# Kernel optimization log

Hardware: AMD Instinct MI355X
Metric: run time of the kernel (lower is better)

Reference implementation:

```python
import jax, jax.numpy as jnp
import numpy as np

N, E = 50000, 400000
HID, EDGE, NRBF = 128, 16, 32
CUTOFF = 5.0
EPS = 1e-8


def setup_inputs() -> dict:
    key = jax.random.key(0)
    ks = jax.random.split(key, 16)
    s = lambda fan_in: 1.0 / np.sqrt(fan_in)
    mlp_in = 3 * HID + NRBF + EDGE  # 432
    return {
        "h": jax.random.normal(ks[0], (N, HID), jnp.float32),
        "vec": jax.random.normal(ks[1], (N, 3, HID), jnp.float32),
        "coord": jax.random.normal(ks[2], (N, 3), jnp.float32),
        "edge_index": jax.random.randint(ks[3], (2, E), 0, N, jnp.int32),
        "edge_attr": jax.random.normal(ks[4], (E, EDGE), jnp.float32),
        "Wvp": jax.random.normal(ks[5], (HID, 3 * HID), jnp.float32) * s(HID),
        "W1": jax.random.normal(ks[6], (mlp_in, HID), jnp.float32) * s(mlp_in),
        "b1": jnp.zeros((HID,), jnp.float32),
        "W2": jax.random.normal(ks[7], (HID, HID), jnp.float32) * s(HID),
        "b2": jnp.zeros((HID,), jnp.float32),
        "W3": jax.random.normal(ks[8], (HID, 3 * HID), jnp.float32) * s(HID),
        "b3": jnp.zeros((3 * HID,), jnp.float32),
        "Wop": jax.random.normal(ks[9], (HID, 3 * HID), jnp.float32) * s(HID),
        "bop": jnp.zeros((3 * HID,), jnp.float32),
    }


def _rbf(d):
    # Gaussian smearing: centers on linspace(0, cutoff, n_rbf)
    offsets = jnp.linspace(0.0, CUTOFF, NRBF, dtype=d.dtype)
    coeff = -0.5 / (offsets[1] - offsets[0]) ** 2
    return jnp.exp(coeff * (d[:, None] - offsets) ** 2)  # [E, NRBF]


def reference(h, vec, coord, edge_index, edge_attr,
              Wvp, W1, b1, W2, b2, W3, b3, Wop, bop):
    row, col = edge_index[0], edge_index[1]
    x_ij = coord[row] - coord[col]                          # [E,3]
    d = jnp.sqrt(jnp.sum(x_ij * x_ij, axis=-1) + EPS)       # stable_norm
    d_ij = _rbf(d)                                          # [E,NRBF]

    vecp = jnp.einsum('nvh,hk->nvk', vec, Wvp)              # [N,3,3H]
    vec1, vec2, vec3 = jnp.split(vecp, 3, axis=-1)          # each [N,3,H]
    vec_dot = jnp.sum(vec1 * vec2, axis=1)                  # [N,H]

    cross = jnp.sum(vec1[row] * vec2[col], axis=1)          # [E,H]
    mlp_in = jnp.concatenate([h[row], h[col], d_ij, cross, edge_attr], axis=-1)
    x = jax.nn.silu(mlp_in @ W1 + b1)
    x = jax.nn.silu(x @ W2 + b2)
    msg = x @ W3 + b3                                       # [E,3H]
    msg_h, msg_v, msg_x = jnp.split(msg, 3, axis=1)

    h_aggr = jax.ops.segment_sum(msg_h, row, num_segments=N)           # [N,H]
    vec_msg = vec3[col] * msg_v[:, None, :] + msg_x[:, None, :] * x_ij[:, :, None]
    vec_aggr = jax.ops.segment_sum(vec_msg, row, num_segments=N)       # [N,3,H]

    o = h_aggr @ Wop + bop
    o1, o2, o3 = jnp.split(o, 3, axis=1)
    dh = vec_dot * o2 + o3
    dvec = vec3 * o1[:, None, :] + vec_aggr
    return dh, dvec
```

## Files before the change

### kernel.cpp

```cpp
#include <hip/hip_runtime.h>
#include <math.h>

constexpr int NN    = 50000;
constexpr int NE    = 400000;
constexpr int HID   = 128;

constexpr size_t OFF_VECP12 = 0;
constexpr size_t OFF_BUN  = 38400000;
constexpr size_t OFF_HAGG = 64000000;
constexpr size_t OFF_WT   = 83200000;
constexpr size_t OFF_PERM = 83421184;
constexpr size_t OFF_DEG  = 83821184;
constexpr size_t OFF_CUR  = 83871184;
constexpr size_t WS_FLOATS = 83921184;

constexpr size_t O_HWH = 0;
constexpr size_t O_HWL = 32768;
constexpr size_t O_W1H = 65536;
constexpr size_t O_W1L = 90112;
constexpr size_t O_W2H = 114688;
constexpr size_t O_W2L = 131072;
constexpr size_t O_W3H = 147456;
constexpr size_t O_W3L = 196608;
constexpr size_t O_VPH = 245760;
constexpr size_t O_VPL = 294912;
constexpr size_t O_OPH = 344064;
constexpr size_t O_OPL = 393216;

typedef __attribute__((ext_vector_type(8))) short short8;
typedef __attribute__((ext_vector_type(4))) float f32x4;

__device__ __forceinline__ short f2bf_rne(float f) {
    unsigned u = __float_as_uint(f);
    u += 0x7fffu + ((u >> 16) & 1u);
    return (short)(u >> 16);
}
__device__ __forceinline__ float bf2f(short h) {
    return __uint_as_float(((unsigned)(unsigned short)h) << 16);
}
__device__ __forceinline__ void split8(const float* t, short8& ah, short8& al) {
#pragma unroll
    for (int j = 0; j < 8; ++j) {
        short hi = f2bf_rne(t[j]);
        ah[j] = hi;
        al[j] = f2bf_rne(t[j] - bf2f(hi));
    }
}
__device__ __forceinline__ f32x4 mfma4(short8 ah, short8 al, short8 bh, short8 bl, f32x4 c) {
    c = __builtin_amdgcn_mfma_f32_16x16x32_bf16(ah, bh, c, 0, 0, 0);
    c = __builtin_amdgcn_mfma_f32_16x16x32_bf16(al, bh, c, 0, 0, 0);
    c = __builtin_amdgcn_mfma_f32_16x16x32_bf16(ah, bl, c, 0, 0, 0);
    c = __builtin_amdgcn_mfma_f32_16x16x32_bf16(al, bl, c, 0, 0, 0);
    return c;
}

#define VLOAD8(dst, src) do { \
    *(float4*)&(dst)[0] = *(const float4*)(src); \
    *(float4*)&(dst)[4] = *(const float4*)((src) + 4); } while (0)

__global__ void misc_kernel(const float* __restrict__ W1, const float* __restrict__ W2,
                            const float* __restrict__ W3, const float* __restrict__ Wvp,
                            const float* __restrict__ Wop, short* __restrict__ wt,
                            const int* __restrict__ eidx, int* __restrict__ deg,
                            float* __restrict__ hagg, float* __restrict__ dvec)
{
    const int bid = blockIdx.x;
    const int idx = bid * 256 + threadIdx.x;
    {
        int n = idx >> 7, k = idx & 127;
        hagg[idx] = 0.f;
        size_t db = (size_t)n * 384 + k;
        dvec[db] = 0.f; dvec[db + 128] = 0.f; dvec[db + 256] = 0.f;
    }
    if (bid < 864) {
        float v; size_t oh, ol;
        if (idx < 32768) {
            int j = idx >> 7, k = idx & 127;
            v = (j < 128) ? W1[(size_t)k * 128 + j] : W1[(size_t)(128 + k) * 128 + (j - 128)];
            oh = O_HWH + idx; ol = O_HWL + idx;
        } else if (idx < 57344) {
            int l = idx - 32768; int n = l / 192, k = l - n * 192;
            int r = (k < 128) ? (288 + k) : (k < 160) ? (256 + k - 128) : (k < 176) ? (416 + k - 160) : -1;
            v = (r < 0) ? 0.f : W1[(size_t)r * 128 + n];
            oh = O_W1H + l; ol = O_W1L + l;
        } else if (idx < 73728) {
            int l = idx - 57344; int n = l >> 7, k = l & 127;
            v = W2[(size_t)k * 128 + n];
            oh = O_W2H + l; ol = O_W2L + l;
        } else if (idx < 122880) {
            int l = idx - 73728; int n = l >> 7, k = l & 127;
            v = W3[(size_t)k * 384 + n];
            oh = O_W3H + l; ol = O_W3L + l;
        } else if (idx < 172032) {
            int l = idx - 122880; int n = l >> 7, k = l & 127;
            v = Wvp[(size_t)k * 384 + n];
            oh = O_VPH + l; ol = O_VPL + l;
        } else {
            int l = idx - 172032; int n = l >> 7, k = l & 127;
            v = Wop[(size_t)k * 384 + n];
            oh = O_OPH + l; ol = O_OPL + l;
        }
        short hi = f2bf_rne(v);
        wt[oh] = hi;
        wt[ol] = f2bf_rne(v - bf2f(hi));
    }
    if (bid < 1563 && idx < NE)
        atomicAdd(&deg[eidx[idx]], 1);
}

__global__ void __launch_bounds__(1024)
sort_scan(const int* __restrict__ deg, int* __restrict__ cursor)
{
    __shared__ int part[1024];
    const int tid = threadIdx.x;
    const int base = tid * 49;
    int s = 0;
#pragma unroll 7
    for (int j = 0; j < 49; ++j) {
        int i = base + j;
        if (i < NN) s += deg[i];
    }
    part[tid] = s;
    __syncthreads();
    for (int off = 1; off < 1024; off <<= 1) {
        int v = (tid >= off) ? part[tid - off] : 0;
        __syncthreads();
        part[tid] += v;
        __syncthreads();
    }
    int run = part[tid] - s;
    for (int j = 0; j < 49; ++j) {
        int i = base + j;
        if (i < NN) { cursor[i] = run; run += deg[i]; }
    }
}

__global__ void sort_scatter(const int* __restrict__ eidx, int* __restrict__ cursor,
                             int* __restrict__ perm)
{
    int e = blockIdx.x * 256 + threadIdx.x;
    if (e < NE) {
        int pos = atomicAdd(&cursor[eidx[e]], 1);
        perm[pos] = e;
    }
}

__global__ void __launch_bounds__(256, 3)
gemm_vp(const float* __restrict__ A, int M,
        const short* __restrict__ wh, const short* __restrict__ wl,
        float* __restrict__ vecp12, short* __restrict__ bun)
{
    const int tid = threadIdx.x, wave = tid >> 6, lane = tid & 63;
    const int m = lane & 15, kg = lane >> 4;
    const int gm0 = blockIdx.x * 32;
    const int nb = wave * 96;
    const f32x4 zf = {0.f, 0.f, 0.f, 0.f};
    f32x4 acc[2][6];
#pragma unroll
    for (int mt = 0; mt < 2; ++mt)
#pragma unroll
        for (int tt = 0; tt < 6; ++tt) acc[mt][tt] = zf;

    for (int ks = 0; ks < 4; ++ks) {
        short8 ah[2], al[2];
#pragma unroll
        for (int mt = 0; mt < 2; ++mt) {
            int r = gm0 + mt * 16 + m;
            if (r >= M) r = M - 1;
            float tmp[8];
            VLOAD8(tmp, A + (size_t)r * 128 + ks * 32 + kg * 8);
            split8(tmp, ah[mt], al[mt]);
        }
#pragma unroll
        for (int tt = 0; tt < 6; ++tt) {
            size_t wo = (size_t)(nb + tt * 16 + m) * 128 + ks * 32 + kg * 8;
            short8 bh = *(const short8*)(wh + wo);
            short8 bl = *(const short8*)(wl + wo);
#pragma unroll
            for (int mt = 0; mt < 2; ++mt)
                acc[mt][tt] = mfma4(ah[mt], al[mt], bh, bl, acc[mt][tt]);
        }
    }
#pragma unroll
    for (int mt = 0; mt < 2; ++mt)
#pragma unroll
        for (int r = 0; r < 4; ++r) {
            int row = gm0 + mt * 16 + kg * 4 + r;
            if (row >= M) continue;
            int n = row / 3, v = row - n * 3;
            size_t fb = (size_t)n * 768 + (size_t)v * 256;
            size_t b2 = (size_t)n * 1024 + (size_t)v * 128;
            size_t b3 = (size_t)n * 1024 + 384 + (size_t)v * 128;
#pragma unroll
            for (int tt = 0; tt < 6; ++tt) {
                int col = nb + tt * 16 + m;
                float val = acc[mt][tt][r];
                int seg = col >> 7, k = col & 127;
                if (seg == 0) {
                    vecp12[fb + k] = val;
                } else if (seg == 1) {
                    vecp12[fb + 128 + k] = val;
                    bun[b2 + k] = f2bf_rne(val);
                } else {
                    bun[b3 + k] = f2bf_rne(val);
                }
            }
        }
}

__global__ void __launch_bounds__(256, 3)
gemm_hw(const float* __restrict__ A, int M,
        const short* __restrict__ wh, const short* __restrict__ wl,
        short* __restrict__ bun)
{
    const int tid = threadIdx.x, wave = tid >> 6, lane = tid & 63;
    const int m = lane & 15, kg = lane >> 4;
    const int gm0 = blockIdx.x * 32;
    const int nb = wave * 64;
    const f32x4 zf = {0.f, 0.f, 0.f, 0.f};
    f32x4 acc[2][4];
#pragma unroll
    for (int mt = 0; mt < 2; ++mt)
#pragma unroll
        for (int tt = 0; tt < 4; ++tt) acc[mt][tt] = zf;

    for (int ks = 0; ks < 4; ++ks) {
        short8 ah[2], al[2];
#pragma unroll
        for (int mt = 0; mt < 2; ++mt) {
            int r = gm0 + mt * 16 + m;
            if (r >= M) r = M - 1;
            float tmp[8];
            VLOAD8(tmp, A + (size_t)r * 128 + ks * 32 + kg * 8);
            split8(tmp, ah[mt], al[mt]);
        }
#pragma unroll
        for (int tt = 0; tt < 4; ++tt) {
            size_t wo = (size_t)(nb + tt * 16 + m) * 128 + ks * 32 + kg * 8;
            short8 bh = *(const short8*)(wh + wo);
            short8 bl = *(const short8*)(wl + wo);
#pragma unroll
            for (int mt = 0; mt < 2; ++mt)
                acc[mt][tt] = mfma4(ah[mt], al[mt], bh, bl, acc[mt][tt]);
        }
    }
#pragma unroll
    for (int mt = 0; mt < 2; ++mt)
#pragma unroll
        for (int r = 0; r < 4; ++r) {
            int row = gm0 + mt * 16 + kg * 4 + r;
            if (row >= M) continue;
#pragma unroll
            for (int tt = 0; tt < 4; ++tt) {
                int col = nb + tt * 16 + m;
                bun[(size_t)row * 1024 + 768 + col] = f2bf_rne(acc[mt][tt][r]);
            }
        }
}

__global__ void __launch_bounds__(256, 3)
gemm_fin(const float* __restrict__ hagg, const float* __restrict__ vecp12,
         const short* __restrict__ bun,
         const short* __restrict__ wh, const short* __restrict__ wl,
         const float* __restrict__ bop, float* __restrict__ dh,
         float* __restrict__ dvec, int M)
{
    const int tid = threadIdx.x, wave = tid >> 6, lane = tid & 63;
    const int m = lane & 15, kg = lane >> 4;
    const int gm0 = blockIdx.x * 32;
    const int nb = wave * 32;
    const f32x4 zf = {0.f, 0.f, 0.f, 0.f};
    f32x4 acc[2][6];
#pragma unroll
    for (int mt = 0; mt < 2; ++mt)
#pragma unroll
        for (int t = 0; t < 6; ++t) acc[mt][t] = zf;

    for (int ks = 0; ks < 4; ++ks) {
        short8 ah[2], al[2];
#pragma unroll
        for (int mt = 0; mt < 2; ++mt) {
            int r = gm0 + mt * 16 + m;
            if (r >= M) r = M - 1;
            float tmp[8];
            VLOAD8(tmp, hagg + (size_t)r * 128 + ks * 32 + kg * 8);
            split8(tmp, ah[mt], al[mt]);
        }
#pragma unroll
        for (int seg = 0; seg < 3; ++seg)
#pragma unroll
            for (int tt = 0; tt < 2; ++tt) {
                size_t wo = (size_t)(seg * 128 + nb + tt * 16 + m) * 128 + ks * 32 + kg * 8;
                short8 bh = *(const short8*)(wh + wo);
                short8 bl = *(const short8*)(wl + wo);
#pragma unroll
                for (int mt = 0; mt < 2; ++mt)
                    acc[mt][seg * 2 + tt] = mfma4(ah[mt], al[mt], bh, bl, acc[mt][seg * 2 + tt]);
            }
    }
    float bo[3][2];
#pragma unroll
    for (int seg = 0; seg < 3; ++seg)
#pragma unroll
        for (int tt = 0; tt < 2; ++tt) bo[seg][tt] = bop[seg * 128 + nb + tt * 16 + m];

#pragma unroll
    for (int mt = 0; mt < 2; ++mt)
#pragma unroll
        for (int r = 0; r < 4; ++r) {
            int row = gm0 + mt * 16 + kg * 4 + r;
            if (row >= M) continue;
            size_t b = (size_t)row * 768;
            size_t bb = (size_t)row * 1024 + 384;
#pragma unroll
            for (int tt = 0; tt < 2; ++tt) {
                int k = nb + tt * 16 + m;
                float o1 = acc[mt][0 * 2 + tt][r] + bo[0][tt];
                float o2 = acc[mt][1 * 2 + tt][r] + bo[1][tt];
                float o3 = acc[mt][2 * 2 + tt][r] + bo[2][tt];
                float vd = vecp12[b + k]       * vecp12[b + 128 + k]
                         + vecp12[b + 256 + k] * vecp12[b + 384 + k]
                         + vecp12[b + 512 + k] * vecp12[b + 640 + k];
                dh[(size_t)row * 128 + k] = vd * o2 + o3;
                size_t db = (size_t)row * 384 + k;
                dvec[db]       += bf2f(bun[bb + k])       * o1;
                dvec[db + 128] += bf2f(bun[bb + 128 + k]) * o1;
                dvec[db + 256] += bf2f(bun[bb + 256 + k]) * o1;
            }
        }
}

__global__ void __launch_bounds__(256, 4)
edge_kernel(const float* __restrict__ vecp12, const short* __restrict__ bun,
            const float* __restrict__ coord, const int* __restrict__ eidx,
            const float* __restrict__ eattr, const short* __restrict__ wt,
            const int* __restrict__ perm,
            const float* __restrict__ b1, const float* __restrict__ b2,
            const float* __restrict__ b3,
            float* __restrict__ hagg, float* __restrict__ dvec)
{
    __shared__ __align__(16) unsigned char smem[34816];
    short (*xh)[136]  = (short(*)[136])(&smem[0]);
    short (*xl)[136]  = (short(*)[136])(&smem[17408]);
    __shared__ int   s_row[64], s_col[64], s_es[64];
    __shared__ float s_xij[64][3];
    __shared__ float s_d[64];

    const int nwg = gridDim.x;
    const int q8 = nwg >> 3, r8 = nwg & 7;
    const int xcd = blockIdx.x & 7, loc = blockIdx.x >> 3;
    const int lb = (xcd < r8 ? xcd * (q8 + 1) : r8 * (q8 + 1) + (xcd - r8) * q8) + loc;

    const int tid = threadIdx.x;
    const int wave = tid >> 6, lane = tid & 63;
    const int m = lane & 15, kg = lane >> 4;
    const int nb = wave * 32;
    const int eb = lb * 64;
    const int be = tid >> 2;
    const int bq = (tid & 3) * 8;

    if (tid < 64) {
        int es = perm[eb + tid];
        int r = eidx[es], c = eidx[NE + es];
        s_es[tid] = es; s_row[tid] = r; s_col[tid] = c;
        float x0 = coord[r * 3 + 0] - coord[c * 3 + 0];
        float x1 = coord[r * 3 + 1] - coord[c * 3 + 1];
        float x2 = coord[r * 3 + 2] - coord[c * 3 + 2];
        s_xij[tid][0] = x0; s_xij[tid][1] = x1; s_xij[tid][2] = x2;
        s_d[tid] = sqrtf(x0 * x0 + x1 * x1 + x2 * x2 + 1e-8f);
    }
    __syncthreads();

    const f32x4 zf = {0.f, 0.f, 0.f, 0.f};
    const float delta = 5.0f / 31.0f;
    const float coeff = -0.5f / (delta * delta);
    const int brow = s_row[be], bcol = s_col[be], bes = s_es[be];

    float pA[8], pC[8], pE[8];
    short8 bB, bD, bF;
    auto issue = [&](int ks) {
        if (ks < 4) {
            int kk = ks * 32 + bq;
            const float* vr = vecp12 + (size_t)brow * 768 + kk;
            const short* vc = bun + (size_t)bcol * 1024 + kk;
            VLOAD8(pA, vr); VLOAD8(pC, vr + 256); VLOAD8(pE, vr + 512);
            bB = *(const short8*)(vc);
            bD = *(const short8*)(vc + 128);
            bF = *(const short8*)(vc + 256);
        } else if (ks == 5) {
            if (bq < 16) VLOAD8(pA, eattr + (size_t)bes * 16 + bq);
        }
    };
    auto commit = [&](int ks, int buf) {
        short (*cabh)[40] = (short(*)[40])(&smem[(size_t)buf * 5120]);
        short (*cabl)[40] = (short(*)[40])(&smem[10240 + (size_t)buf * 5120]);
        float tmp[8];
        if (ks < 4) {
#pragma unroll
            for (int j = 0; j < 8; ++j)
                tmp[j] = pA[j] * bf2f(bB[j]) + pC[j] * bf2f(bD[j]) + pE[j] * bf2f(bF[j]);
        } else if (ks == 4) {
            float dd = s_d[be];
#pragma unroll
            for (int j = 0; j < 8; ++j) {
                float x = dd - (float)(bq + j) * delta;
                tmp[j] = __expf(coeff * x * x);
            }
        } else {
#pragma unroll
            for (int j = 0; j < 8; ++j) tmp[j] = (bq < 16) ? pA[j] : 0.f;
        }
        short8 sh, sl; split8(tmp, sh, sl);
        *(short8*)&cabh[be][bq] = sh;
        *(short8*)&cabl[be][bq] = sl;
    };

    f32x4 acc[4][2];
#pragma unroll
    for (int mt = 0; mt < 4; ++mt) { acc[mt][0] = zf; acc[mt][1] = zf; }

    issue(0); commit(0, 0);
    __syncthreads();
    for (int ks = 0; ks < 6; ++ks) {
        if (ks < 5) issue(ks + 1);
        const short (*rabh)[40] = (const short(*)[40])(&smem[(size_t)(ks & 1) * 5120]);
        const short (*rabl)[40] = (const short(*)[40])(&smem[10240 + (size_t)(ks & 1) * 5120]);
        short8 ah4[4], al4[4];
#pragma unroll
        for (int mt = 0; mt < 4; ++mt) {
            ah4[mt] = *(const short8*)&rabh[mt * 16 + m][kg * 8];
            al4[mt] = *(const short8*)&rabl[mt * 16 + m][kg * 8];
        }
#pragma unroll
        for (int tt = 0; tt < 2; ++tt) {
            size_t wo = (size_t)(nb + tt * 16 + m) * 192 + ks * 32 + kg * 8;
            short8 bh = *(const short8*)(wt + O_W1H + wo);
            short8 bl = *(const short8*)(wt + O_W1L + wo);
#pragma unroll
            for (int mt = 0; mt < 4; ++mt)
                acc[mt][tt] = mfma4(ah4[mt], al4[mt], bh, bl, acc[mt][tt]);
        }
        if (ks < 5) commit(ks + 1, (ks + 1) & 1);
        __syncthreads();
    }

    {
        float b1v[2] = { b1[nb + m], b1[nb + 16 + m] };
#pragma unroll
        for (int mt = 0; mt < 4; ++mt) {
            float hb[4][4];
#pragma unroll
            for (int r = 0; r < 4; ++r) {
                int e = mt * 16 + kg * 4 + r;
                const short* hr = bun + (size_t)s_row[e] * 1024 + 768;
                const short* hc = bun + (size_t)s_col[e] * 1024 + 896;
                hb[r][0] = bf2f(hr[nb + m]);      hb[r][1] = bf2f(hc[nb + m]);
                hb[r][2] = bf2f(hr[nb + 16 + m]); hb[r][3] = bf2f(hc[nb + 16 + m]);
            }
#pragma unroll
            for (int r = 0; r < 4; ++r) {
                int e = mt * 16 + kg * 4 + r;
#pragma unroll
                for (int tt = 0; tt < 2; ++tt) {
                    int n = nb + tt * 16 + m;
                    float v = acc[mt][tt][r] + hb[r][tt * 2] + hb[r][tt * 2 + 1] + b1v[tt];
                    float sv = v * __builtin_amdgcn_rcpf(1.f + __expf(-v));
                    short hi = f2bf_rne(sv);
                    xh[e][n] = hi;
                    xl[e][n] = f2bf_rne(sv - bf2f(hi));
                }
            }
        }
    }
    __syncthreads();

#pragma unroll
    for (int mt = 0; mt < 4; ++mt) { acc[mt][0] = zf; acc[mt][1] = zf; }
    for (int ks = 0; ks < 4; ++ks) {
        short8 ah4[4], al4[4];
#pragma unroll
        for (int mt = 0; mt < 4; ++mt) {
            ah4[mt] = *(const short8*)&xh[mt * 16 + m][ks * 32 + kg * 8];
            al4[mt] = *(const short8*)&xl[mt * 16 + m][ks * 32 + kg * 8];
        }
#pragma unroll
        for (int tt = 0; tt < 2; ++tt) {
            size_t wo = (size_t)(nb + tt * 16 + m) * 128 + ks * 32 + kg * 8;
            short8 bh = *(const short8*)(wt + O_W2H + wo);
            short8 bl = *(const short8*)(wt + O_W2L + wo);
#pragma unroll
            for (int mt = 0; mt < 4; ++mt)
                acc[mt][tt] = mfma4(ah4[mt], al4[mt], bh, bl, acc[mt][tt]);
        }
    }
    {
        float b2v[2] = { b2[nb + m], b2[nb + 16 + m] };
#pragma unroll
        for (int mt = 0; mt < 4; ++mt)
#pragma unroll
            for (int tt = 0; tt < 2; ++tt)
#pragma unroll
                for (int r = 0; r < 4; ++r) {
                    float v = acc[mt][tt][r] + b2v[tt];
                    acc[mt][tt][r] = v * __builtin_amdgcn_rcpf(1.f + __expf(-v));
                }
    }
    __syncthreads();
#pragma unroll
    for (int mt = 0; mt < 4; ++mt)
#pragma unroll
        for (int tt = 0; tt < 2; ++tt)
#pragma unroll
            for (int r = 0; r < 4; ++r) {
                int e = mt * 16 + kg * 4 + r;
                int n = nb + tt * 16 + m;
                float sv = acc[mt][tt][r];
                short hi = f2bf_rne(sv);
                xh[e][n] = hi;
                xl[e][n] = f2bf_rne(sv - bf2f(hi));
            }
    __syncthreads();

    float msgv[4][2][4];
    for (int c = 0; c < 3; ++c) {
        f32x4 a3[4][2];
#pragma unroll
        for (int mt = 0; mt < 4; ++mt) { a3[mt][0] = zf; a3[mt][1] = zf; }
        for (int ks = 0; ks < 4; ++ks) {
            short8 ah4[4], al4[4];
#pragma unroll
            for (int mt = 0; mt < 4; ++mt) {
                ah4[mt] = *(const short8*)&xh[mt * 16 + m][ks * 32 + kg * 8];
                al4[mt] = *(const short8*)&xl[mt * 16 + m][ks * 32 + kg * 8];
            }
#pragma unroll
            for (int tt = 0; tt < 2; ++tt) {
                size_t wo = (size_t)(c * 128 + nb + tt * 16 + m) * 128 + ks * 32 + kg * 8;
                short8 bh = *(const short8*)(wt + O_W3H + wo);
                short8 bl = *(const short8*)(wt + O_W3L + wo);
#pragma unroll
                for (int mt = 0; mt < 4; ++mt)
                    a3[mt][tt] = mfma4(ah4[mt], al4[mt], bh, bl, a3[mt][tt]);
            }
        }
        float bv[2] = { b3[c * 128 + nb + m], b3[c * 128 + nb + 16 + m] };
        const int n0 = nb + m, n1 = nb + 16 + m;
        if (c == 0) {
            int cur = s_row[kg * 4];
            float s0 = 0.f, s1 = 0.f;
#pragma unroll
            for (int mt = 0; mt < 4; ++mt)
#pragma unroll
                for (int r = 0; r < 4; ++r) {
                    int rr = s_row[mt * 16 + kg * 4 + r];
                    float v0 = a3[mt][0][r] + bv[0];
                    float v1 = a3[mt][1][r] + bv[1];
                    if (rr != cur) {
                        atomicAdd(&hagg[(size_t)cur * 128 + n0], s0);
                        atomicAdd(&hagg[(size_t)cur * 128 + n1], s1);
                        cur = rr; s0 = 0.f; s1 = 0.f;
                    }
                    s0 += v0; s1 += v1;
                }
            atomicAdd(&hagg[(size_t)cur * 128 + n0], s0);
            atomicAdd(&hagg[(size_t)cur * 128 + n1], s1);
        } else if (c == 1) {
#pragma unroll
            for (int mt = 0; mt < 4; ++mt)
#pragma unroll
                for (int tt = 0; tt < 2; ++tt)
#pragma unroll
                    for (int r = 0; r < 4; ++r)
                        msgv[mt][tt][r] = a3[mt][tt][r] + bv[tt];
        } else {
            int cur = s_row[kg * 4];
            float sd[6] = {0.f, 0.f, 0.f, 0.f, 0.f, 0.f};
#pragma unroll
            for (int mt = 0; mt < 4; ++mt) {
                float v3b[4][6];
#pragma unroll
                for (int r = 0; r < 4; ++r) {
                    int e = mt * 16 + kg * 4 + r;
                    const short* v3 = bun + (size_t)s_col[e] * 1024 + 384;
                    v3b[r][0] = bf2f(v3[n0]); v3b[r][1] = bf2f(v3[128 + n0]); v3b[r][2] = bf2f(v3[256 + n0]);
                    v3b[r][3] = bf2f(v3[n1]); v3b[r][4] = bf2f(v3[128 + n1]); v3b[r][5] = bf2f(v3[256 + n1]);
                }
#pragma unroll
                for (int r = 0; r < 4; ++r) {
                    int e = mt * 16 + kg * 4 + r;
                    int rr = s_row[e];
                    if (rr != cur) {
                        float* dst = dvec + (size_t)cur * 384;
                        atomicAdd(dst + n0,       sd[0]);
                        atomicAdd(dst + 128 + n0, sd[1]);
                        atomicAdd(dst + 256 + n0, sd[2]);
                        atomicAdd(dst + n1,       sd[3]);
                        atomicAdd(dst + 128 + n1, sd[4]);
                        atomicAdd(dst + 256 + n1, sd[5]);
                        cur = rr;
#pragma unroll
                        for (int q = 0; q < 6; ++q) sd[q] = 0.f;
                    }
                    const float xj0 = s_xij[e][0], xj1 = s_xij[e][1], xj2 = s_xij[e][2];
                    float mx0 = a3[mt][0][r] + bv[0], mx1 = a3[mt][1][r] + bv[1];
                    float mv0 = msgv[mt][0][r],       mv1 = msgv[mt][1][r];
                    sd[0] += v3b[r][0] * mv0 + xj0 * mx0;
                    sd[1] += v3b[r][1] * mv0 + xj1 * mx0;
                    sd[2] += v3b[r][2] * mv0 + xj2 * mx0;
                    sd[3] += v3b[r][3] * mv1 + xj0 * mx1;
                    sd[4] += v3b[r][4] * mv1 + xj1 * mx1;
                    sd[5] += v3b[r][5] * mv1 + xj2 * mx1;
                }
            }
            float* dst = dvec + (size_t)cur * 384;
            atomicAdd(dst + n0,       sd[0]);
            atomicAdd(dst + 128 + n0, sd[1]);
            atomicAdd(dst + 256 + n0, sd[2]);
            atomicAdd(dst + n1,       sd[3]);
            atomicAdd(dst + 128 + n1, sd[4]);
            atomicAdd(dst + 256 + n1, sd[5]);
        }
    }
}

extern "C" void kernel_launch(void* const* d_in, const int* in_sizes, int n_in,
                              void* d_out, int out_size, void* d_ws, size_t ws_size,
                              hipStream_t stream)
{
    const float* h     = (const float*)d_in[0];
    const float* vec   = (const float*)d_in[1];
    const float* coord = (const float*)d_in[2];
    const int*   eidx  = (const int*)  d_in[3];
    const float* eattr = (const float*)d_in[4];
    const float* Wvp   = (const float*)d_in[5];
    const float* W1    = (const float*)d_in[6];
    const float* b1    = (const float*)d_in[7];
    const float* W2    = (const float*)d_in[8];
    const float* b2    = (const float*)d_in[9];
    const float* W3    = (const float*)d_in[10];
    const float* b3    = (const float*)d_in[11];
    const float* Wop   = (const float*)d_in[12];
    const float* bop   = (const float*)d_in[13];

    if (ws_size < WS_FLOATS * sizeof(float)) return;

    float* ws     = (float*)d_ws;
    float* vecp12 = ws + OFF_VECP12;
    short* bun    = (short*)(ws + OFF_BUN);
    float* hagg   = ws + OFF_HAGG;
    short* wt     = (short*)(ws + OFF_WT);
    int*   perm   = (int*)(ws + OFF_PERM);
    int*   deg    = (int*)(ws + OFF_DEG);
    int*   cur    = (int*)(ws + OFF_CUR);
    float* dh     = (float*)d_out;
    float* dvec   = (float*)d_out + (size_t)NN * HID;

    dim3 b256(256);
    hipMemsetAsync(deg, 0, NN * sizeof(int), stream);
    misc_kernel<<<25000, b256, 0, stream>>>(W1, W2, W3, Wvp, Wop, wt, eidx, deg, hagg, dvec);
    sort_scan<<<1, 1024, 0, stream>>>(deg, cur);
    sort_scatter<<<1563, b256, 0, stream>>>(eidx, cur, perm);
    gemm_vp<<<4688, b256, 0, stream>>>(vec, 150000, wt + O_VPH, wt + O_VPL, vecp12, bun);
    gemm_hw<<<1563, b256, 0, stream>>>(h, 50000, wt + O_HWH, wt + O_HWL, bun);
    edge_kernel<<<6250, b256, 0, stream>>>(vecp12, bun, coord, eidx, eattr, wt, perm,
                                           b1, b2, b3, hagg, dvec);
    gemm_fin<<<1563, b256, 0, stream>>>(hagg, vecp12, bun, wt + O_OPH, wt + O_OPL,
                                        bop, dh, dvec, 50000);
}
```

Before: 1.289 ms.

## Drop low-bf16 activation split, halving MFMAs and shared memory in all GEMMs

Activations are now rounded to a single bf16 instead of a hi/lo split, so each GEMM tile issues two MFMAs instead of four; only the weights keep the hi/lo pair. The fp32 copy of vec2 is no longer stored, and vec_dot reads the bf16 copy from the bundle, which shrinks workspace traffic. Edge-kernel shared memory is halved and launch bounds are raised from 4 to 8 blocks per SM to increase occupancy. The cost is lower accuracy on activations, which may push the error near the tolerance.

Result: slower. 1.706 ms (+32.4%).

```diff
diff --git a/kernel.cpp b/kernel.cpp
--- a/kernel.cpp
+++ b/kernel.cpp
@@ -5,9 +5,9 @@
 constexpr int NE    = 400000;
 constexpr int HID   = 128;
 
-constexpr size_t OFF_VECP12 = 0;
-constexpr size_t OFF_BUN  = 38400000;
-constexpr size_t OFF_HAGG = 64000000;
+constexpr size_t OFF_VECP1 = 0;
+constexpr size_t OFF_BUN  = 19200000;
+constexpr size_t OFF_HAGG = 44800000;
 constexpr size_t OFF_WT   = 83200000;
 constexpr size_t OFF_PERM = 83421184;
 constexpr size_t OFF_DEG  = 83821184;
@@ -38,19 +38,15 @@
 __device__ __forceinline__ float bf2f(short h) {
     return __uint_as_float(((unsigned)(unsigned short)h) << 16);
 }
-__device__ __forceinline__ void split8(const float* t, short8& ah, short8& al) {
-#pragma unroll
-    for (int j = 0; j < 8; ++j) {
-        short hi = f2bf_rne(t[j]);
-        ah[j] = hi;
-        al[j] = f2bf_rne(t[j] - bf2f(hi));
-    }
-}
-__device__ __forceinline__ f32x4 mfma4(short8 ah, short8 al, short8 bh, short8 bl, f32x4 c) {
-    c = __builtin_amdgcn_mfma_f32_16x16x32_bf16(ah, bh, c, 0, 0, 0);
-    c = __builtin_amdgcn_mfma_f32_16x16x32_bf16(al, bh, c, 0, 0, 0);
-    c = __builtin_amdgcn_mfma_f32_16x16x32_bf16(ah, bl, c, 0, 0, 0);
-    c = __builtin_amdgcn_mfma_f32_16x16x32_bf16(al, bl, c, 0, 0, 0);
+__device__ __forceinline__ short8 tobf8(const float* t) {
+    short8 r;
+#pragma unroll
+    for (int j = 0; j < 8; ++j) r[j] = f2bf_rne(t[j]);
+    return r;
+}
+__device__ __forceinline__ f32x4 mfma2(short8 a, short8 bh, short8 bl, f32x4 c) {
+    c = __builtin_amdgcn_mfma_f32_16x16x32_bf16(a, bh, c, 0, 0, 0);
+    c = __builtin_amdgcn_mfma_f32_16x16x32_bf16(a, bl, c, 0, 0, 0);
     return c;
 }
 
@@ -148,7 +144,7 @@
 __global__ void __launch_bounds__(256, 3)
 gemm_vp(const float* __restrict__ A, int M,
         const short* __restrict__ wh, const short* __restrict__ wl,
-        float* __restrict__ vecp12, short* __restrict__ bun)
+        float* __restrict__ vecp1, short* __restrict__ bun)
 {
     const int tid = threadIdx.x, wave = tid >> 6, lane = tid & 63;
     const int m = lane & 15, kg = lane >> 4;
@@ -162,14 +158,14 @@
         for (int tt = 0; tt < 6; ++tt) acc[mt][tt] = zf;
 
     for (int ks = 0; ks < 4; ++ks) {
-        short8 ah[2], al[2];
+        short8 ah[2];
 #pragma unroll
         for (int mt = 0; mt < 2; ++mt) {
             int r = gm0 + mt * 16 + m;
             if (r >= M) r = M - 1;
             float tmp[8];
             VLOAD8(tmp, A + (size_t)r * 128 + ks * 32 + kg * 8);
-            split8(tmp, ah[mt], al[mt]);
+            ah[mt] = tobf8(tmp);
         }
 #pragma unroll
         for (int tt = 0; tt < 6; ++tt) {
@@ -178,7 +174,7 @@
             short8 bl = *(const short8*)(wl + wo);
 #pragma unroll
             for (int mt = 0; mt < 2; ++mt)
-                acc[mt][tt] = mfma4(ah[mt], al[mt], bh, bl, acc[mt][tt]);
+                acc[mt][tt] = mfma2(ah[mt], bh, bl, acc[mt][tt]);
         }
     }
 #pragma unroll
@@ -188,7 +184,7 @@
             int row = gm0 + mt * 16 + kg * 4 + r;
             if (row >= M) continue;
             int n = row / 3, v = row - n * 3;
-            size_t fb = (size_t)n * 768 + (size_t)v * 256;
+            size_t fb = (size_t)n * 384 + (size_t)v * 128;
             size_t b2 = (size_t)n * 1024 + (size_t)v * 128;
             size_t b3 = (size_t)n * 1024 + 384 + (size_t)v * 128;
 #pragma unroll
@@ -196,14 +192,9 @@
                 int col = nb + tt * 16 + m;
                 float val = acc[mt][tt][r];
                 int seg = col >> 7, k = col & 127;
-                if (seg == 0) {
-                    vecp12[fb + k] = val;
-                } else if (seg == 1) {
-                    vecp12[fb + 128 + k] = val;
-                    bun[b2 + k] = f2bf_rne(val);
-                } else {
-                    bun[b3 + k] = f2bf_rne(val);
-                }
+                if (seg == 0)      vecp1[fb + k] = val;
+                else if (seg == 1) bun[b2 + k] = f2bf_rne(val);
+                else               bun[b3 + k] = f2bf_rne(val);
             }
         }
 }
@@ -225,14 +216,14 @@
         for (int tt = 0; tt < 4; ++tt) acc[mt][tt] = zf;
 
     for (int ks = 0; ks < 4; ++ks) {
-        short8 ah[2], al[2];
+        short8 ah[2];
 #pragma unroll
         for (int mt = 0; mt < 2; ++mt) {
             int r = gm0 + mt * 16 + m;
             if (r >= M) r = M - 1;
             float tmp[8];
             VLOAD8(tmp, A + (size_t)r * 128 + ks * 32 + kg * 8);
-            split8(tmp, ah[mt], al[mt]);
+            ah[mt] = tobf8(tmp);
         }
 #pragma unroll
         for (int tt = 0; tt < 4; ++tt) {
@@ -241,7 +232,7 @@
             short8 bl = *(const short8*)(wl + wo);
 #pragma unroll
             for (int mt = 0; mt < 2; ++mt)
-                acc[mt][tt] = mfma4(ah[mt], al[mt], bh, bl, acc[mt][tt]);
+                acc[mt][tt] = mfma2(ah[mt], bh, bl, acc[mt][tt]);
         }
     }
 #pragma unroll
@@ -259,7 +250,7 @@
 }
 
 __global__ void __launch_bounds__(256, 3)
-gemm_fin(const float* __restrict__ hagg, const float* __restrict__ vecp12,
+gemm_fin(const float* __restrict__ hagg, const float* __restrict__ vecp1,
          const short* __restrict__ bun,
          const short* __restrict__ wh, const short* __restrict__ wl,
          const float* __restrict__ bop, float* __restrict__ dh,
@@ -277,14 +268,14 @@
         for (int t = 0; t < 6; ++t) acc[mt][t] = zf;
 
     for (int ks = 0; ks < 4; ++ks) {
-        short8 ah[2], al[2];
+        short8 ah[2];
 #pragma unroll
         for (int mt = 0; mt < 2; ++mt) {
             int r = gm0 + mt * 16 + m;
             if (r >= M) r = M - 1;
             float tmp[8];
             VLOAD8(tmp, hagg + (size_t)r * 128 + ks * 32 + kg * 8);
-            split8(tmp, ah[mt], al[mt]);
+            ah[mt] = tobf8(tmp);
         }
 #pragma unroll
         for (int seg = 0; seg < 3; ++seg)
@@ -295,7 +286,7 @@
                 short8 bl = *(const short8*)(wl + wo);
 #pragma unroll
                 for (int mt = 0; mt < 2; ++mt)
-                    acc[mt][seg * 2 + tt] = mfma4(ah[mt], al[mt], bh, bl, acc[mt][seg * 2 + tt]);
+                    acc[mt][seg * 2 + tt] = mfma2(ah[mt], bh, bl, acc[mt][seg * 2 + tt]);
             }
     }
     float bo[3][2];
@@ -310,7 +301,8 @@
         for (int r = 0; r < 4; ++r) {
             int row = gm0 + mt * 16 + kg * 4 + r;
             if (row >= M) continue;
-            size_t b = (size_t)row * 768;
+            size_t b = (size_t)row * 384;
+            size_t b2 = (size_t)row * 1024;
             size_t bb = (size_t)row * 1024 + 384;
 #pragma unroll
             for (int tt = 0; tt < 2; ++tt) {
@@ -318,9 +310,9 @@
                 float o1 = acc[mt][0 * 2 + tt][r] + bo[0][tt];
                 float o2 = acc[mt][1 * 2 + tt][r] + bo[1][tt];
                 float o3 = acc[mt][2 * 2 + tt][r] + bo[2][tt];
-                float vd = vecp12[b + k]       * vecp12[b + 128 + k]
-                         + vecp12[b + 256 + k] * vecp12[b + 384 + k]
-                         + vecp12[b + 512 + k] * vecp12[b + 640 + k];
+                float vd = vecp1[b + k]       * bf2f(bun[b2 + k])
+                         + vecp1[b + 128 + k] * bf2f(bun[b2 + 128 + k])
+                         + vecp1[b + 256 + k] * bf2f(bun[b2 + 256 + k]);
                 dh[(size_t)row * 128 + k] = vd * o2 + o3;
                 size_t db = (size_t)row * 384 + k;
                 dvec[db]       += bf2f(bun[bb + k])       * o1;
@@ -330,8 +322,8 @@
         }
 }
 
-__global__ void __launch_bounds__(256, 4)
-edge_kernel(const float* __restrict__ vecp12, const short* __restrict__ bun,
+__global__ void __launch_bounds__(256, 8)
+edge_kernel(const float* __restrict__ vecp1, const short* __restrict__ bun,
             const float* __restrict__ coord, const int* __restrict__ eidx,
             const float* __restrict__ eattr, const short* __restrict__ wt,
             const int* __restrict__ perm,
@@ -339,9 +331,8 @@
             const float* __restrict__ b3,
             float* __restrict__ hagg, float* __restrict__ dvec)
 {
-    __shared__ __align__(16) unsigned char smem[34816];
+    __shared__ __align__(16) unsigned char smem[17408];
     short (*xh)[136]  = (short(*)[136])(&smem[0]);
-    short (*xl)[136]  = (short(*)[136])(&smem[17408]);
     __shared__ int   s_row[64], s_col[64], s_es[64];
     __shared__ float s_xij[64][3];
     __shared__ float s_d[64];
@@ -381,9 +372,9 @@
     auto issue = [&](int ks) {
         if (ks < 4) {
             int kk = ks * 32 + bq;
-            const float* vr = vecp12 + (size_t)brow * 768 + kk;
+            const float* vr = vecp1 + (size_t)brow * 384 + kk;
             const short* vc = bun + (size_t)bcol * 1024 + kk;
-            VLOAD8(pA, vr); VLOAD8(pC, vr + 256); VLOAD8(pE, vr + 512);
+            VLOAD8(pA, vr); VLOAD8(pC, vr + 128); VLOAD8(pE, vr + 256);
             bB = *(const short8*)(vc);
             bD = *(const short8*)(vc + 128);
             bF = *(const short8*)(vc + 256);
@@ -392,8 +383,7 @@
         }
     };
     auto commit = [&](int ks, int buf) {
-        short (*cabh)[40] = (short(*)[40])(&smem[(size_t)buf * 5120]);
-        short (*cabl)[40] = (short(*)[40])(&smem[10240 + (size_t)buf * 5120]);
+        short (*cab)[40] = (short(*)[40])(&smem[(size_t)buf * 5120]);
         float tmp[8];
         if (ks < 4) {
 #pragma unroll
@@ -410,9 +400,7 @@
 #pragma unroll
             for (int j = 0; j < 8; ++j) tmp[j] = (bq < 16) ? pA[j] : 0.f;
         }
-        short8 sh, sl; split8(tmp, sh, sl);
-        *(short8*)&cabh[be][bq] = sh;
-        *(short8*)&cabl[be][bq] = sl;
+        *(short8*)&cab[be][bq] = tobf8(tmp);
     };
 
     f32x4 acc[4][2];
@@ -423,14 +411,11 @@
     __syncthreads();
     for (int ks = 0; ks < 6; ++ks) {
         if (ks < 5) issue(ks + 1);
-        const short (*rabh)[40] = (const short(*)[40])(&smem[(size_t)(ks & 1) * 5120]);
-        const short (*rabl)[40] = (const short(*)[40])(&smem[10240 + (size_t)(ks & 1) * 5120]);
-        short8 ah4[4], al4[4];
-#pragma unroll
-        for (int mt = 0; mt < 4; ++mt) {
-            ah4[mt] = *(const short8*)&rabh[mt * 16 + m][kg * 8];
-            al4[mt] = *(const short8*)&rabl[mt * 16 + m][kg * 8];
-        }
+        const short (*rab)[40] = (const short(*)[40])(&smem[(size_t)(ks & 1) * 5120]);
+        short8 ah4[4];
+#pragma unroll
+        for (int mt = 0; mt < 4; ++mt)
+            ah4[mt] = *(const short8*)&rab[mt * 16 + m][kg * 8];
 #pragma unroll
         for (int tt = 0; tt < 2; ++tt) {
             size_t wo = (size_t)(nb + tt * 16 + m) * 192 + ks * 32 + kg * 8;
@@ -438,7 +423,7 @@
             short8 bl = *(const short8*)(wt + O_W1L + wo);
 #pragma unroll
             for (int mt = 0; mt < 4; ++mt)
-                acc[mt][tt] = mfma4(ah4[mt], al4[mt], bh, bl, acc[mt][tt]);
+                acc[mt][tt] = mfma2(ah4[mt], bh, bl, acc[mt][tt]);
         }
         if (ks < 5) commit(ks + 1, (ks + 1) & 1);
         __syncthreads();
@@ -465,9 +450,7 @@
                     int n = nb + tt * 16 + m;
                     float v = acc[mt][tt][r] + hb[r][tt * 2] + hb[r][tt * 2 + 1] + b1v[tt];
                     float sv = v * __builtin_amdgcn_rcpf(1.f + __expf(-v));
-                    short hi = f2bf_rne(sv);
-                    xh[e][n] = hi;
-                    xl[e][n] = f2bf_rne(sv - bf2f(hi));
+                    xh[e][n] = f2bf_rne(sv);
                 }
             }
         }
@@ -477,12 +460,10 @@
 #pragma unroll
     for (int mt = 0; mt < 4; ++mt) { acc[mt][0] = zf; acc[mt][1] = zf; }
     for (int ks = 0; ks < 4; ++ks) {
-        short8 ah4[4], al4[4];
-#pragma unroll
-        for (int mt = 0; mt < 4; ++mt) {
+        short8 ah4[4];
+#pragma unroll
+        for (int mt = 0; mt < 4; ++mt)
             ah4[mt] = *(const short8*)&xh[mt * 16 + m][ks * 32 + kg * 8];
-            al4[mt] = *(const short8*)&xl[mt * 16 + m][ks * 32 + kg * 8];
-        }
 #pragma unroll
         for (int tt = 0; tt < 2; ++tt) {
             size_t wo = (size_t)(nb + tt * 16 + m) * 128 + ks * 32 + kg * 8;
@@ -490,7 +471,7 @@
             short8 bl = *(const short8*)(wt + O_W2L + wo);
 #pragma unroll
             for (int mt = 0; mt < 4; ++mt)
-                acc[mt][tt] = mfma4(ah4[mt], al4[mt], bh, bl, acc[mt][tt]);
+                acc[mt][tt] = mfma2(ah4[mt], bh, bl, acc[mt][tt]);
         }
     }
     {
@@ -514,10 +495,7 @@
             for (int r = 0; r < 4; ++r) {
                 int e = mt * 16 + kg * 4 + r;
                 int n = nb + tt * 16 + m;
-                float sv = acc[mt][tt][r];
-                short hi = f2bf_rne(sv);
-                xh[e][n] = hi;
-                xl[e][n] = f2bf_rne(sv - bf2f(hi));
+                xh[e][n] = f2bf_rne(acc[mt][tt][r]);
             }
     __syncthreads();
 
@@ -527,12 +505,10 @@
 #pragma unroll
         for (int mt = 0; mt < 4; ++mt) { a3[mt][0] = zf; a3[mt][1] = zf; }
         for (int ks = 0; ks < 4; ++ks) {
-            short8 ah4[4], al4[4];
-#pragma unroll
-            for (int mt = 0; mt < 4; ++mt) {
+            short8 ah4[4];
+#pragma unroll
+            for (int mt = 0; mt < 4; ++mt)
                 ah4[mt] = *(const short8*)&xh[mt * 16 + m][ks * 32 + kg * 8];
-                al4[mt] = *(const short8*)&xl[mt * 16 + m][ks * 32 + kg * 8];
-            }
 #pragma unroll
             for (int tt = 0; tt < 2; ++tt) {
                 size_t wo = (size_t)(c * 128 + nb + tt * 16 + m) * 128 + ks * 32 + kg * 8;
@@ -540,7 +516,7 @@
                 short8 bl = *(const short8*)(wt + O_W3L + wo);
 #pragma unroll
                 for (int mt = 0; mt < 4; ++mt)
-                    a3[mt][tt] = mfma4(ah4[mt], al4[mt], bh, bl, a3[mt][tt]);
+                    a3[mt][tt] = mfma2(ah4[mt], bh, bl, a3[mt][tt]);
             }
         }
         float bv[2] = { b3[c * 128 + nb + m], b3[c * 128 + nb + 16 + m] };
@@ -644,26 +620,26 @@
 
     if (ws_size < WS_FLOATS * sizeof(float)) return;
 
-    float* ws     = (float*)d_ws;
-    float* vecp12 = ws + OFF_VECP12;
-    short* bun    = (short*)(ws + OFF_BUN);
-    float* hagg   = ws + OFF_HAGG;
-    short* wt     = (short*)(ws + OFF_WT);
-    int*   perm   = (int*)(ws + OFF_PERM);
-    int*   deg    = (int*)(ws + OFF_DEG);
-    int*   cur    = (int*)(ws + OFF_CUR);
-    float* dh     = (float*)d_out;
-    float* dvec   = (float*)d_out + (size_t)NN * HID;
+    float* ws    = (float*)d_ws;
+    float* vecp1 = ws + OFF_VECP1;
+    short* bun   = (short*)(ws + OFF_BUN);
+    float* hagg  = ws + OFF_HAGG;
+    short* wt    = (short*)(ws + OFF_WT);
+    int*   perm  = (int*)(ws + OFF_PERM);
+    int*   deg   = (int*)(ws + OFF_DEG);
+    int*   cur   = (int*)(ws + OFF_CUR);
+    float* dh    = (float*)d_out;
+    float* dvec  = (float*)d_out + (size_t)NN * HID;
 
     dim3 b256(256);
     hipMemsetAsync(deg, 0, NN * sizeof(int), stream);
     misc_kernel<<<25000, b256, 0, stream>>>(W1, W2, W3, Wvp, Wop, wt, eidx, deg, hagg, dvec);
     sort_scan<<<1, 1024, 0, stream>>>(deg, cur);
     sort_scatter<<<1563, b256, 0, stream>>>(eidx, cur, perm);
-    gemm_vp<<<4688, b256, 0, stream>>>(vec, 150000, wt + O_VPH, wt + O_VPL, vecp12, bun);
+    gemm_vp<<<4688, b256, 0, stream>>>(vec, 150000, wt + O_VPH, wt + O_VPL, vecp1, bun);
     gemm_hw<<<1563, b256, 0, stream>>>(h, 50000, wt + O_HWH, wt + O_HWL, bun);
-    edge_kernel<<<6250, b256, 0, stream>>>(vecp12, bun, coord, eidx, eattr, wt, perm,
+    edge_kernel<<<6250, b256, 0, stream>>>(vecp1, bun, coord, eidx, eattr, wt, perm,
                                            b1, b2, b3, hagg, dvec);
-    gemm_fin<<<1563, b256, 0, stream>>>(hagg, vecp12, bun, wt + O_OPH, wt + O_OPL,
+    gemm_fin<<<1563, b256, 0, stream>>>(hagg, vecp1, bun, wt + O_OPH, wt + O_OPL,
                                         bop, dh, dvec, 50000);
 }
```
